# Kernel tuning notes

Measured on AMD Instinct MI355X. Metric: run time of the kernel, lower is better.

The kernel has to match this reference:

```python
import jax, jax.numpy as jnp
import numpy as np

NUM_HEADS = 16


def setup_inputs() -> dict:
    key = jax.random.key(0)
    ks = jax.random.split(key, 6)
    B, N, M, D = 4, 2048, 2048, 1024
    s = 1.0 / np.sqrt(D)
    return {
        "inputs": jax.random.normal(ks[0], (B, N, D), dtype=jnp.float32),
        "encoderOutputs": jax.random.normal(ks[1], (B, M, D), dtype=jnp.float32),
        "wq": jax.random.normal(ks[2], (D, D), dtype=jnp.float32) * s,
        "wk": jax.random.normal(ks[3], (D, D), dtype=jnp.float32) * s,
        "wv": jax.random.normal(ks[4], (D, D), dtype=jnp.float32) * s,
        "wo": jax.random.normal(ks[5], (D, D), dtype=jnp.float32) * s,
    }


def reference(inputs, encoderOutputs, wq, wk, wv, wo):
    B, N, D = inputs.shape
    M = encoderOutputs.shape[1]
    H = NUM_HEADS
    hd = D // H
    # Linear layers (no bias; torch Linear computes x @ W.T, weights here stored as [dOut,dIn])
    q = (inputs @ wq.T).reshape(B, N, H, hd).transpose(0, 2, 1, 3)        # [B,H,N,hd]
    k = (encoderOutputs @ wk.T).reshape(B, M, H, hd).transpose(0, 2, 1, 3)  # [B,H,M,hd]
    v = (encoderOutputs @ wv.T).reshape(B, M, H, hd).transpose(0, 2, 1, 3)  # [B,H,M,hd]
    scores = jnp.einsum('bhnd,bhmd->bhnm', q, k) / jnp.sqrt(jnp.float32(hd))
    attn = jax.nn.softmax(scores, axis=-1)  # dropout p=0.0 -> identity
    ctx = jnp.einsum('bhnm,bhmd->bhnd', attn, v)
    ctx = ctx.transpose(0, 2, 1, 3).reshape(B, N, D)
    return ctx @ wo.T
```

## Files before the change

### kernel.cpp

```cpp
#include <hip/hip_runtime.h>
#include <hip/hip_bf16.h>


typedef __attribute__((ext_vector_type(8))) short bf16x8;
typedef __attribute__((ext_vector_type(4))) float f32x4;
typedef __attribute__((ext_vector_type(16))) float f32x16;
typedef __attribute__((ext_vector_type(4))) unsigned short u16x4;
typedef __attribute__((ext_vector_type(4))) unsigned int u32x4;

#define SEQ 2048
#define H_ 16

static __device__ __forceinline__ unsigned short f2bf(float f) {
  unsigned int u = __float_as_uint(f);
  u += 0x7fffu + ((u >> 16) & 1u);
  return (unsigned short)(u >> 16);
}

static __device__ __forceinline__ void gload16(const void* g, void* l) {
  __builtin_amdgcn_global_load_lds((const __attribute__((address_space(1))) void*)g,
                                   (__attribute__((address_space(3))) void*)l, 16, 0, 0);
}

__global__ __launch_bounds__(256) void k_cvt_w(const float* __restrict__ wq, const float* __restrict__ wk,
    const float* __restrict__ wv, const float* __restrict__ wo,
    unsigned short* __restrict__ Wqb, unsigned short* __restrict__ Wkb,
    unsigned short* __restrict__ Wvb, unsigned short* __restrict__ Wob) {
  int i = blockIdx.x * 256 + threadIdx.x;
  const float* src; unsigned short* dst; int off;
  if (i < 262144)       { src = wq; dst = Wqb; off = i; }
  else if (i < 524288)  { src = wk; dst = Wkb; off = i - 262144; }
  else if (i < 786432)  { src = wv; dst = Wvb; off = i - 524288; }
  else                  { src = wo; dst = Wob; off = i - 786432; }
  float4 v = reinterpret_cast<const float4*>(src)[off];
  u16x4 o;
  o[0] = f2bf(v.x); o[1] = f2bf(v.y); o[2] = f2bf(v.z); o[3] = f2bf(v.w);
  *reinterpret_cast<u16x4*>(dst + (size_t)off * 4) = o;
}

template<int F32A, typename EPI>
static __device__ __forceinline__ void gemm_core(char* __restrict__ smem,
                                                 const void* __restrict__ Av,
                                                 const unsigned short* __restrict__ W,
                                                 int col0, int row0, EPI epi) {
  char* AsB = smem;
  unsigned short* Ws = (unsigned short*)(smem + (F32A ? 16384 : 8192));
  const int tid = threadIdx.x, lane = tid & 63, w = tid >> 6;
  const int wr = w >> 1, wc = w & 1;
  f32x4 acc[4][4];
  for (int i = 0; i < 4; ++i)
    for (int j = 0; j < 4; ++j)
      for (int e = 0; e < 4; ++e) acc[i][j][e] = 0.f;

  size_t aoff[F32A ? 4 : 2];
  int aldso[F32A ? 4 : 2];
  if (F32A) {
#pragma unroll
    for (int h = 0; h < 4; ++h) {
      int ch = tid + h * 256;
      int row = ch >> 3, colb = (ch & 7) << 4;
      int ge = (colb ^ ((row & 7) << 4)) >> 2;
      aoff[h] = (size_t)(row0 + row) * 1024 + ge;
      aldso[h] = ch * 16;
    }
  } else {
#pragma unroll
    for (int h = 0; h < 2; ++h) {
      int ch = tid + h * 256;
      int row = ch >> 2, c8 = (ch & 3) * 8;
      aoff[h] = (size_t)(row0 + row) * 1024 + c8;
      aldso[h] = ch * 16;
    }
  }
  size_t woff[2];
  int wldso[2];
#pragma unroll
  for (int h = 0; h < 2; ++h) {
    int ch = tid + h * 256;
    int row = ch >> 2, c8 = (ch & 3) * 8;
    woff[h] = (size_t)(col0 + row) * 1024 + c8;
    wldso[h] = ch * 16;
  }

  const int fr = lane & 15, ko = (lane >> 4) * 8;
  for (int k0 = 0; k0 < 1024; k0 += 32) {
    __syncthreads();
    if (F32A) {
      const float* Af = (const float*)Av;
#pragma unroll
      for (int h = 0; h < 4; ++h)
        gload16(Af + aoff[h] + k0, AsB + aldso[h]);
    } else {
      const unsigned short* Ab = (const unsigned short*)Av;
#pragma unroll
      for (int h = 0; h < 2; ++h)
        gload16(Ab + aoff[h] + k0, AsB + aldso[h]);
    }
#pragma unroll
    for (int h = 0; h < 2; ++h)
      gload16(W + woff[h] + k0, (char*)Ws + wldso[h]);
    __syncthreads();

    bf16x8 af[4], bfr[4];
#pragma unroll
    for (int mi = 0; mi < 4; ++mi) {
      int r = wr * 64 + mi * 16 + fr;
      if (F32A) {
        int swz = (r & 7) << 4;
        int b0 = r * 128 + ko * 4;
        f32x4 x0 = *(const f32x4*)(AsB + ((b0) ^ swz));
        f32x4 x1 = *(const f32x4*)(AsB + ((b0 + 16) ^ swz));
        unsigned pw[4];
        asm("v_cvt_pk_bf16_f32 %0, %1, %2" : "=v"(pw[0]) : "v"(x0[0]), "v"(x0[1]));
        asm("v_cvt_pk_bf16_f32 %0, %1, %2" : "=v"(pw[1]) : "v"(x0[2]), "v"(x0[3]));
        asm("v_cvt_pk_bf16_f32 %0, %1, %2" : "=v"(pw[2]) : "v"(x1[0]), "v"(x1[1]));
        asm("v_cvt_pk_bf16_f32 %0, %1, %2" : "=v"(pw[3]) : "v"(x1[2]), "v"(x1[3]));
        u32x4 fa = { pw[0], pw[1], pw[2], pw[3] };
        af[mi] = __builtin_bit_cast(bf16x8, fa);
      } else {
        af[mi] = *(const bf16x8*)(AsB + (r * 32 + ko) * 2);
      }
    }
#pragma unroll
    for (int ni = 0; ni < 4; ++ni)
      bfr[ni] = *(const bf16x8*)&Ws[(wc * 64 + ni * 16 + fr) * 32 + ko];
#pragma unroll
    for (int mi = 0; mi < 4; ++mi)
#pragma unroll
      for (int ni = 0; ni < 4; ++ni)
        acc[mi][ni] = __builtin_amdgcn_mfma_f32_16x16x32_bf16(af[mi], bfr[ni], acc[mi][ni], 0, 0, 0);
  }
  for (int mi = 0; mi < 4; ++mi)
    for (int ni = 0; ni < 4; ++ni) {
      int r0 = row0 + wr * 64 + mi * 16 + (lane >> 4) * 4;
      int o = col0 + wc * 64 + ni * 16 + (lane & 15);
      epi(r0, o, acc[mi][ni]);
    }
}

static __device__ __forceinline__ void panel_decode(int& col0, int& row0) {
  int lin = blockIdx.x + 8 * blockIdx.y;
  int er = (lin & 7) * 8 + ((lin >> 3) & 7);
  int ec = lin >> 6;
  col0 = ec * 128;
  row0 = er * 128;
}

__global__ __launch_bounds__(256) void k_gemm_qkv(const float* __restrict__ x,
                                                  const float* __restrict__ e,
                                                  const unsigned short* __restrict__ Wqb,
                                                  const unsigned short* __restrict__ Wkb,
                                                  const unsigned short* __restrict__ Wvb,
                                                  unsigned short* __restrict__ Qb,
                                                  unsigned short* __restrict__ Kb,
                                                  unsigned short* __restrict__ Vtg) {
  __shared__ __align__(16) char smem[16384 + 8192];
  const int z = blockIdx.z;
  int col0, row0;
  panel_decode(col0, row0);
  const void* A = (z == 0) ? (const void*)x : (const void*)e;
  const unsigned short* W = (z == 0) ? Wqb : (z == 1) ? Wkb : Wvb;
  if (z == 2) {
    gemm_core<1>(smem, A, W, col0, row0, [&](int r0, int o, f32x4 v) {
      int b = r0 >> 11, n0 = r0 & (SEQ - 1);
      int h = o >> 6, c = o & 63;
      u16x4 o4;
      for (int j = 0; j < 4; ++j) o4[j] = f2bf(v[j]);
      *(u16x4*)&Vtg[(((size_t)(b * H_ + h)) * 64 + c) * SEQ + n0] = o4;
    });
  } else {
    unsigned short* out = (z == 0) ? Qb : Kb;
    const float sc = (z == 0) ? 0.18033688f : 1.0f;
    gemm_core<1>(smem, A, W, col0, row0, [&](int r0, int o, f32x4 v) {
      int b = r0 >> 11, n0 = r0 & (SEQ - 1);
      int h = o >> 6, c = o & 63;
      for (int j = 0; j < 4; ++j)
        out[(((size_t)(b * H_ + h)) * SEQ + n0 + j) * 64 + c] = f2bf(v[j] * sc);
    });
  }
}

__global__ __launch_bounds__(256) void k_gemm_out(const unsigned short* __restrict__ A,
                                                  const unsigned short* __restrict__ W,
                                                  float* __restrict__ out) {
  __shared__ __align__(16) char smem[8192 + 8192];
  int col0, row0;
  panel_decode(col0, row0);
  gemm_core<0>(smem, A, W, col0, row0, [&](int r0, int o, f32x4 v) {
    for (int j = 0; j < 4; ++j)
      out[(size_t)(r0 + j) * 1024 + o] = v[j];
  });
}

static __device__ __forceinline__ int swzaddr(int row, int colb) {
  return row * 128 + (colb ^ ((row & 7) << 4));
}

__global__ __launch_bounds__(512) void k_attn(const unsigned short* __restrict__ Qh,
                                              const unsigned short* __restrict__ Kh,
                                              const unsigned short* __restrict__ Vtg,
                                              unsigned short* __restrict__ CTX) {
  __shared__ __align__(16) char lds[4 * 8192];
  const int tid = threadIdx.x, lane = tid & 63, w = tid >> 6;
  const int hi = lane >> 5, q = lane & 31;
  const int id = blockIdx.x;
  const int bh = (id & 7) * 8 + ((id >> 3) & 7);
  const int qt = id >> 6;
  const size_t kvbase = (size_t)bh * (SEQ * 64);
  const size_t qrow = (size_t)bh * SEQ + qt * 256 + w * 32 + q;
  bf16x8 qf[4];
#pragma unroll
  for (int c = 0; c < 4; ++c)
    qf[c] = *(const bf16x8*)&Qh[qrow * 64 + c * 16 + hi * 8];
  f32x16 oacc0, oacc1, oaccL, fzero;
#pragma unroll
  for (int r = 0; r < 16; ++r) { oacc0[r] = 0.f; oacc1[r] = 0.f; oaccL[r] = 0.f; fzero[r] = 0.f; }
  bf16x8 ones;
#pragma unroll
  for (int r = 0; r < 8; ++r) ones[r] = (short)0x3F80;

  const int sc = tid;
  const int srow = sc >> 3, spb = (sc & 7) << 4;
  const int sge = (spb ^ ((srow & 7) << 4)) >> 1;
  const size_t koff = (size_t)srow * 64 + sge;
  const size_t voff = (size_t)srow * SEQ + sge;
  const int ldso = sc * 16;

#define STAGE(T, BUFO)                                                        \
  {                                                                           \
    gload16(Kh + kvbase + (size_t)(T) * 4096 + koff, lds + (BUFO) + ldso);    \
    gload16(Vtg + kvbase + (size_t)(T) * 64 + voff, lds + (BUFO) + 8192 + ldso); \
  }

  STAGE(0, 0);

  for (int t = 0; t < 32; ++t) {
    __syncthreads();
    const int bo = (t & 1) * 16384;
    char* Kb = lds + bo;
    char* Vb = lds + bo + 8192;
    if (t + 1 < 32) STAGE(t + 1, ((t + 1) & 1) * 16384);

    f32x16 s0, s1;
    __builtin_amdgcn_s_setprio(1);
    {
      bf16x8 kf0 = *(const bf16x8*)(Kb + swzaddr(q, 0 * 32 + hi * 16));
      bf16x8 kf1 = *(const bf16x8*)(Kb + swzaddr(32 + q, 0 * 32 + hi * 16));
      s0 = __builtin_amdgcn_mfma_f32_32x32x16_bf16(kf0, qf[0], fzero, 0, 0, 0);
      s1 = __builtin_amdgcn_mfma_f32_32x32x16_bf16(kf1, qf[0], fzero, 0, 0, 0);
    }
#pragma unroll
    for (int c = 1; c < 4; ++c) {
      bf16x8 kf0 = *(const bf16x8*)(Kb + swzaddr(q, c * 32 + hi * 16));
      bf16x8 kf1 = *(const bf16x8*)(Kb + swzaddr(32 + q, c * 32 + hi * 16));
      s0 = __builtin_amdgcn_mfma_f32_32x32x16_bf16(kf0, qf[c], s0, 0, 0, 0);
      s1 = __builtin_amdgcn_mfma_f32_32x32x16_bf16(kf1, qf[c], s1, 0, 0, 0);
    }
    __builtin_amdgcn_s_setprio(0);

    bf16x8 pfrag[4];

#define SOFT_PACK(SREG, FA, FB)                                               \
    {                                                                         \
      float pa[16];                                                           \
      _Pragma("unroll")                                                       \
      for (int r = 0; r < 16; ++r) pa[r] = __builtin_amdgcn_exp2f(SREG[r]);   \
      unsigned pw[8];                                                         \
      _Pragma("unroll")                                                       \
      for (int i = 0; i < 8; ++i)                                             \
        asm("v_cvt_pk_bf16_f32 %0, %1, %2" : "=v"(pw[i])                      \
            : "v"(pa[2 * i]), "v"(pa[2 * i + 1]));                            \
      asm("v_permlane32_swap_b32 %0, %1" : "+v"(pw[0]), "+v"(pw[2]));         \
      asm("v_permlane32_swap_b32 %0, %1" : "+v"(pw[1]), "+v"(pw[3]));         \
      asm("v_permlane32_swap_b32 %0, %1" : "+v"(pw[4]), "+v"(pw[6]));         \
      asm("v_permlane32_swap_b32 %0, %1" : "+v"(pw[5]), "+v"(pw[7]));         \
      u32x4 fa = { pw[0], pw[1], pw[2], pw[3] };                              \
      u32x4 fb = { pw[4], pw[5], pw[6], pw[7] };                              \
      FA = __builtin_bit_cast(bf16x8, fa);                                    \
      FB = __builtin_bit_cast(bf16x8, fb);                                    \
    }

    SOFT_PACK(s0, pfrag[0], pfrag[1])
    SOFT_PACK(s1, pfrag[2], pfrag[3])
#undef SOFT_PACK

    __builtin_amdgcn_s_setprio(1);
#pragma unroll
    for (int kk = 0; kk < 4; ++kk) {
      bf16x8 vf0 = *(const bf16x8*)(Vb + swzaddr(q, kk * 32 + hi * 16));
      bf16x8 vf1 = *(const bf16x8*)(Vb + swzaddr(32 + q, kk * 32 + hi * 16));
      oacc0 = __builtin_amdgcn_mfma_f32_32x32x16_bf16(vf0, pfrag[kk], oacc0, 0, 0, 0);
      oacc1 = __builtin_amdgcn_mfma_f32_32x32x16_bf16(vf1, pfrag[kk], oacc1, 0, 0, 0);
      oaccL = __builtin_amdgcn_mfma_f32_32x32x16_bf16(ones, pfrag[kk], oaccL, 0, 0, 0);
    }
    __builtin_amdgcn_s_setprio(0);
  }
#undef STAGE

  const float inv = 1.0f / oaccL[0];
  const int b = bh >> 4, h = bh & 15;
  const size_t orow = ((size_t)b * SEQ + qt * 256 + w * 32 + q) * 1024 + h * 64;
#pragma unroll
  for (int g = 0; g < 4; ++g) {
    u16x4 o0, o1;
#pragma unroll
    for (int j = 0; j < 4; ++j) {
      o0[j] = f2bf(oacc0[g * 4 + j] * inv);
      o1[j] = f2bf(oacc1[g * 4 + j] * inv);
    }
    *(u16x4*)&CTX[orow + g * 8 + hi * 4] = o0;
    *(u16x4*)&CTX[orow + 32 + g * 8 + hi * 4] = o1;
  }
}

extern "C" void kernel_launch(void* const* d_in, const int* in_sizes, int n_in,
                              void* d_out, int out_size, void* d_ws, size_t ws_size,
                              hipStream_t stream) {
  const float* x  = (const float*)d_in[0];
  const float* e  = (const float*)d_in[1];
  const float* wq = (const float*)d_in[2];
  const float* wk = (const float*)d_in[3];
  const float* wv = (const float*)d_in[4];
  const float* wo = (const float*)d_in[5];
  unsigned short* Wqb = (unsigned short*)d_ws;
  unsigned short* Wkb = Wqb + 1048576;
  unsigned short* Wvb = Wkb + 1048576;
  unsigned short* Wob = Wvb + 1048576;
  unsigned short* Qb  = Wob + 1048576;
  unsigned short* Kb  = Qb + 8388608;
  unsigned short* Vtg = Kb + 8388608;
  unsigned short* Cb  = Vtg + 8388608;

  k_cvt_w<<<4096, 256, 0, stream>>>(wq, wk, wv, wo, Wqb, Wkb, Wvb, Wob);

  k_gemm_qkv<<<dim3(8, 64, 3), 256, 0, stream>>>(x, e, Wqb, Wkb, Wvb, Qb, Kb, Vtg);

  k_attn<<<512, 512, 0, stream>>>(Qb, Kb, Vtg, Cb);

  k_gemm_out<<<dim3(8, 64), 256, 0, stream>>>(Cb, Wob, (float*)d_out);
}
```

Baseline: 192.7 us.

## Double-buffer GEMM LDS tiles and XOR-swizzle bf16 tile layout

```diff
diff --git a/kernel.cpp b/kernel.cpp
--- a/kernel.cpp
+++ b/kernel.cpp
@@ -43,8 +43,8 @@
                                                  const void* __restrict__ Av,
                                                  const unsigned short* __restrict__ W,
                                                  int col0, int row0, EPI epi) {
-  char* AsB = smem;
-  unsigned short* Ws = (unsigned short*)(smem + (F32A ? 16384 : 8192));
+  constexpr int ASZ = F32A ? 16384 : 8192;
+  constexpr int BUF = ASZ + 8192;
   const int tid = threadIdx.x, lane = tid & 63, w = tid >> 6;
   const int wr = w >> 1, wc = w & 1;
   f32x4 acc[4][4];
@@ -67,8 +67,8 @@
 #pragma unroll
     for (int h = 0; h < 2; ++h) {
       int ch = tid + h * 256;
-      int row = ch >> 2, c8 = (ch & 3) * 8;
-      aoff[h] = (size_t)(row0 + row) * 1024 + c8;
+      int row = ch >> 2, s = ch & 3;
+      aoff[h] = (size_t)(row0 + row) * 1024 + (size_t)((s ^ (row & 3)) * 8);
       aldso[h] = ch * 16;
     }
   }
@@ -77,29 +77,40 @@
 #pragma unroll
   for (int h = 0; h < 2; ++h) {
     int ch = tid + h * 256;
-    int row = ch >> 2, c8 = (ch & 3) * 8;
-    woff[h] = (size_t)(col0 + row) * 1024 + c8;
+    int row = ch >> 2, s = ch & 3;
+    woff[h] = (size_t)(col0 + row) * 1024 + (size_t)((s ^ (row & 3)) * 8);
     wldso[h] = ch * 16;
   }
 
+#define GSTAGE(K0, BUFO)                                                      \
+  {                                                                           \
+    if (F32A) {                                                               \
+      const float* Af_ = (const float*)Av;                                    \
+      _Pragma("unroll")                                                       \
+      for (int h = 0; h < 4; ++h)                                             \
+        gload16(Af_ + aoff[h] + (K0), smem + (BUFO) + aldso[h]);              \
+    } else {                                                                  \
+      const unsigned short* Ab_ = (const unsigned short*)Av;                  \
+      _Pragma("unroll")                                                       \
+      for (int h = 0; h < 2; ++h)                                             \
+        gload16(Ab_ + aoff[h] + (K0), smem + (BUFO) + aldso[h]);              \
+    }                                                                         \
+    _Pragma("unroll")                                                         \
+    for (int h = 0; h < 2; ++h)                                               \
+      gload16(W + woff[h] + (K0), smem + (BUFO) + ASZ + wldso[h]);            \
+  }
+
   const int fr = lane & 15, ko = (lane >> 4) * 8;
-  for (int k0 = 0; k0 < 1024; k0 += 32) {
+  const int slot = lane >> 4;
+
+  GSTAGE(0, 0);
+
+  for (int kt = 0; kt < 32; ++kt) {
     __syncthreads();
-    if (F32A) {
-      const float* Af = (const float*)Av;
-#pragma unroll
-      for (int h = 0; h < 4; ++h)
-        gload16(Af + aoff[h] + k0, AsB + aldso[h]);
-    } else {
-      const unsigned short* Ab = (const unsigned short*)Av;
-#pragma unroll
-      for (int h = 0; h < 2; ++h)
-        gload16(Ab + aoff[h] + k0, AsB + aldso[h]);
-    }
-#pragma unroll
-    for (int h = 0; h < 2; ++h)
-      gload16(W + woff[h] + k0, (char*)Ws + wldso[h]);
-    __syncthreads();
+    const int bo = (kt & 1) * BUF;
+    const char* AsB = smem + bo;
+    const char* WsB = smem + bo + ASZ;
+    if (kt + 1 < 32) GSTAGE((kt + 1) * 32, ((kt + 1) & 1) * BUF);
 
     bf16x8 af[4], bfr[4];
 #pragma unroll
@@ -118,18 +129,22 @@
         u32x4 fa = { pw[0], pw[1], pw[2], pw[3] };
         af[mi] = __builtin_bit_cast(bf16x8, fa);
       } else {
-        af[mi] = *(const bf16x8*)(AsB + (r * 32 + ko) * 2);
+        af[mi] = *(const bf16x8*)(AsB + r * 64 + ((slot ^ (r & 3)) * 16));
       }
     }
 #pragma unroll
-    for (int ni = 0; ni < 4; ++ni)
-      bfr[ni] = *(const bf16x8*)&Ws[(wc * 64 + ni * 16 + fr) * 32 + ko];
+    for (int ni = 0; ni < 4; ++ni) {
+      int r = wc * 64 + ni * 16 + fr;
+      bfr[ni] = *(const bf16x8*)(WsB + r * 64 + ((slot ^ (r & 3)) * 16));
+    }
 #pragma unroll
     for (int mi = 0; mi < 4; ++mi)
 #pragma unroll
       for (int ni = 0; ni < 4; ++ni)
         acc[mi][ni] = __builtin_amdgcn_mfma_f32_16x16x32_bf16(af[mi], bfr[ni], acc[mi][ni], 0, 0, 0);
   }
+#undef GSTAGE
+
   for (int mi = 0; mi < 4; ++mi)
     for (int ni = 0; ni < 4; ++ni) {
       int r0 = row0 + wr * 64 + mi * 16 + (lane >> 4) * 4;
@@ -154,7 +169,7 @@
                                                   unsigned short* __restrict__ Qb,
                                                   unsigned short* __restrict__ Kb,
                                                   unsigned short* __restrict__ Vtg) {
-  __shared__ __align__(16) char smem[16384 + 8192];
+  __shared__ __align__(16) char smem[2 * (16384 + 8192)];
   const int z = blockIdx.z;
   int col0, row0;
   panel_decode(col0, row0);
@@ -183,7 +198,7 @@
 __global__ __launch_bounds__(256) void k_gemm_out(const unsigned short* __restrict__ A,
                                                   const unsigned short* __restrict__ W,
                                                   float* __restrict__ out) {
-  __shared__ __align__(16) char smem[8192 + 8192];
+  __shared__ __align__(16) char smem[2 * (8192 + 8192)];
   int col0, row0;
   panel_decode(col0, row0);
   gemm_core<0>(smem, A, W, col0, row0, [&](int r0, int o, f32x4 v) {
```

New measurement: 201.9 us. 4.7% more time.

## Fuse K and V projections into one kernel sharing the encoder A tile

Applied to the files above, without the earlier changes.

```diff
diff --git a/kernel.cpp b/kernel.cpp
--- a/kernel.cpp
+++ b/kernel.cpp
@@ -36,6 +36,14 @@
   u16x4 o;
   o[0] = f2bf(v.x); o[1] = f2bf(v.y); o[2] = f2bf(v.z); o[3] = f2bf(v.w);
   *reinterpret_cast<u16x4*>(dst + (size_t)off * 4) = o;
+}
+
+static __device__ __forceinline__ void panel_decode(int& col0, int& row0) {
+  int lin = blockIdx.x + 8 * blockIdx.y;
+  int er = (lin & 7) * 8 + ((lin >> 3) & 7);
+  int ec = lin >> 6;
+  col0 = ec * 128;
+  row0 = er * 128;
 }
 
 template<int F32A, typename EPI>
@@ -138,46 +146,110 @@
     }
 }
 
-static __device__ __forceinline__ void panel_decode(int& col0, int& row0) {
-  int lin = blockIdx.x + 8 * blockIdx.y;
-  int er = (lin & 7) * 8 + ((lin >> 3) & 7);
-  int ec = lin >> 6;
-  col0 = ec * 128;
-  row0 = er * 128;
-}
-
-__global__ __launch_bounds__(256) void k_gemm_qkv(const float* __restrict__ x,
-                                                  const float* __restrict__ e,
-                                                  const unsigned short* __restrict__ Wqb,
-                                                  const unsigned short* __restrict__ Wkb,
-                                                  const unsigned short* __restrict__ Wvb,
-                                                  unsigned short* __restrict__ Qb,
-                                                  unsigned short* __restrict__ Kb,
-                                                  unsigned short* __restrict__ Vtg) {
+__global__ __launch_bounds__(256) void k_gemm_q(const float* __restrict__ x,
+                                                const unsigned short* __restrict__ Wqb,
+                                                unsigned short* __restrict__ Qb) {
   __shared__ __align__(16) char smem[16384 + 8192];
-  const int z = blockIdx.z;
   int col0, row0;
   panel_decode(col0, row0);
-  const void* A = (z == 0) ? (const void*)x : (const void*)e;
-  const unsigned short* W = (z == 0) ? Wqb : (z == 1) ? Wkb : Wvb;
-  if (z == 2) {
-    gemm_core<1>(smem, A, W, col0, row0, [&](int r0, int o, f32x4 v) {
+  gemm_core<1>(smem, x, Wqb, col0, row0, [&](int r0, int o, f32x4 v) {
+    int b = r0 >> 11, n0 = r0 & (SEQ - 1);
+    int h = o >> 6, c = o & 63;
+    for (int j = 0; j < 4; ++j)
+      Qb[(((size_t)(b * H_ + h)) * SEQ + n0 + j) * 64 + c] = f2bf(v[j] * 0.18033688f);
+  });
+}
+
+__global__ __launch_bounds__(512) void k_gemm_kv(const float* __restrict__ e,
+                                                 const unsigned short* __restrict__ Wkb,
+                                                 const unsigned short* __restrict__ Wvb,
+                                                 unsigned short* __restrict__ Kb,
+                                                 unsigned short* __restrict__ Vtg) {
+  __shared__ __align__(16) char smem[16384 + 8192 + 8192];
+  char* AsB = smem;
+  unsigned short* Ks = (unsigned short*)(smem + 16384);
+  unsigned short* Vs = (unsigned short*)(smem + 24576);
+  const int tid = threadIdx.x, lane = tid & 63, w = tid >> 6;
+  const int ws = w & 3, isV = w >> 2;
+  const int wr = ws >> 1, wc = ws & 1;
+  int col0, row0;
+  panel_decode(col0, row0);
+  f32x4 acc[4][4];
+  for (int i = 0; i < 4; ++i)
+    for (int j = 0; j < 4; ++j)
+      for (int el = 0; el < 4; ++el) acc[i][j][el] = 0.f;
+
+  size_t aoff[2];
+  int aldso[2];
+#pragma unroll
+  for (int h = 0; h < 2; ++h) {
+    int ch = tid + h * 512;
+    int row = ch >> 3, colb = (ch & 7) << 4;
+    int ge = (colb ^ ((row & 7) << 4)) >> 2;
+    aoff[h] = (size_t)(row0 + row) * 1024 + ge;
+    aldso[h] = ch * 16;
+  }
+  size_t woff;
+  int wldso;
+  {
+    int ch = tid;
+    int row = ch >> 2, c8 = (ch & 3) * 8;
+    woff = (size_t)(col0 + row) * 1024 + c8;
+    wldso = ch * 16;
+  }
+
+  const int fr = lane & 15, ko = (lane >> 4) * 8;
+  for (int k0 = 0; k0 < 1024; k0 += 32) {
+    __syncthreads();
+#pragma unroll
+    for (int h = 0; h < 2; ++h)
+      gload16(e + aoff[h] + k0, AsB + aldso[h]);
+    gload16(Wkb + woff + k0, (char*)Ks + wldso);
+    gload16(Wvb + woff + k0, (char*)Vs + wldso);
+    __syncthreads();
+
+    const unsigned short* Wsel = isV ? Vs : Ks;
+    bf16x8 af[4], bfr[4];
+#pragma unroll
+    for (int mi = 0; mi < 4; ++mi) {
+      int r = wr * 64 + mi * 16 + fr;
+      int swz = (r & 7) << 4;
+      int b0 = r * 128 + ko * 4;
+      f32x4 x0 = *(const f32x4*)(AsB + ((b0) ^ swz));
+      f32x4 x1 = *(const f32x4*)(AsB + ((b0 + 16) ^ swz));
+      unsigned pw[4];
+      asm("v_cvt_pk_bf16_f32 %0, %1, %2" : "=v"(pw[0]) : "v"(x0[0]), "v"(x0[1]));
+      asm("v_cvt_pk_bf16_f32 %0, %1, %2" : "=v"(pw[1]) : "v"(x0[2]), "v"(x0[3]));
+      asm("v_cvt_pk_bf16_f32 %0, %1, %2" : "=v"(pw[2]) : "v"(x1[0]), "v"(x1[1]));
+      asm("v_cvt_pk_bf16_f32 %0, %1, %2" : "=v"(pw[3]) : "v"(x1[2]), "v"(x1[3]));
+      u32x4 fa = { pw[0], pw[1], pw[2], pw[3] };
+      af[mi] = __builtin_bit_cast(bf16x8, fa);
+    }
+#pragma unroll
+    for (int ni = 0; ni < 4; ++ni)
+      bfr[ni] = *(const bf16x8*)&Wsel[(wc * 64 + ni * 16 + fr) * 32 + ko];
+#pragma unroll
+    for (int mi = 0; mi < 4; ++mi)
+#pragma unroll
+      for (int ni = 0; ni < 4; ++ni)
+        acc[mi][ni] = __builtin_amdgcn_mfma_f32_16x16x32_bf16(af[mi], bfr[ni], acc[mi][ni], 0, 0, 0);
+  }
+
+  for (int mi = 0; mi < 4; ++mi)
+    for (int ni = 0; ni < 4; ++ni) {
+      int r0 = row0 + wr * 64 + mi * 16 + (lane >> 4) * 4;
+      int o = col0 + wc * 64 + ni * 16 + (lane & 15);
       int b = r0 >> 11, n0 = r0 & (SEQ - 1);
       int h = o >> 6, c = o & 63;
-      u16x4 o4;
-      for (int j = 0; j < 4; ++j) o4[j] = f2bf(v[j]);
-      *(u16x4*)&Vtg[(((size_t)(b * H_ + h)) * 64 + c) * SEQ + n0] = o4;
-    });
-  } else {
-    unsigned short* out = (z == 0) ? Qb : Kb;
-    const float sc = (z == 0) ? 0.18033688f : 1.0f;
-    gemm_core<1>(smem, A, W, col0, row0, [&](int r0, int o, f32x4 v) {
-      int b = r0 >> 11, n0 = r0 & (SEQ - 1);
-      int h = o >> 6, c = o & 63;
-      for (int j = 0; j < 4; ++j)
-        out[(((size_t)(b * H_ + h)) * SEQ + n0 + j) * 64 + c] = f2bf(v[j] * sc);
-    });
-  }
+      if (isV) {
+        u16x4 o4;
+        for (int j = 0; j < 4; ++j) o4[j] = f2bf(acc[mi][ni][j]);
+        *(u16x4*)&Vtg[(((size_t)(b * H_ + h)) * 64 + c) * SEQ + n0] = o4;
+      } else {
+        for (int j = 0; j < 4; ++j)
+          Kb[(((size_t)(b * H_ + h)) * SEQ + n0 + j) * 64 + c] = f2bf(acc[mi][ni][j]);
+      }
+    }
 }
 
 __global__ __launch_bounds__(256) void k_gemm_out(const unsigned short* __restrict__ A,
@@ -333,9 +405,11 @@
 
   k_cvt_w<<<4096, 256, 0, stream>>>(wq, wk, wv, wo, Wqb, Wkb, Wvb, Wob);
 
-  k_gemm_qkv<<<dim3(8, 64, 3), 256, 0, stream>>>(x, e, Wqb, Wkb, Wvb, Qb, Kb, Vtg);
+  dim3 gg(8, 64);
+  k_gemm_kv<<<gg, 512, 0, stream>>>(e, Wkb, Wvb, Kb, Vtg);
+  k_gemm_q<<<gg, 256, 0, stream>>>(x, Wqb, Qb);
 
   k_attn<<<512, 512, 0, stream>>>(Qb, Kb, Vtg, Cb);
 
-  k_gemm_out<<<dim3(8, 64), 256, 0, stream>>>(Cb, Wob, (float*)d_out);
-}
+  k_gemm_out<<<gg, 256, 0, stream>>>(Cb, Wob, (float*)d_out);
+}
```

Measured after the change: 199.9 us. +3.7%, slower.
